# Kernel tuning notes

Hardware: AMD Instinct MI355X
Metric: run time of the kernel (lower is better)

The kernel has to match this reference:

```python
import jax, jax.numpy as jnp
import numpy as np

ITER = 50
HEADS = 8

def _ln(x, g, b, eps=1e-5):
    m = jnp.mean(x, -1, keepdims=True)
    v = jnp.var(x, -1, keepdims=True)
    return (x - m) * jax.lax.rsqrt(v + eps) * g + b

def _glu(x):
    a, b = jnp.split(x, 2, -1)
    return a * jax.nn.sigmoid(b)

def setup_inputs() -> dict:
    key = jax.random.key(0)
    ks = iter(jax.random.split(key, 48))
    B, D, E, M, H, O, NA, NO = 64, 2048, 512, 25, 32, 4096, 512, 512
    def nrm(shape, fan):
        return jax.random.normal(next(ks), shape, jnp.float32) / np.float32(np.sqrt(fan))
    return dict(
        x=jax.random.normal(next(ks), (B, 12, 8, 8), jnp.float32),
        kv_w=nrm((12, E), 12), kv_b=jnp.zeros(E), kv_ln_g=jnp.ones(E), kv_ln_b=jnp.zeros(E),
        q_w=nrm((NA, E), NA), q_b=jnp.zeros(E),
        wq=nrm((E, E), E), wk=nrm((E, E), E), wv=nrm((E, E), E), wo=nrm((E, E), E),
        bq=jnp.zeros(E), bk=jnp.zeros(E), bv=jnp.zeros(E), bo=jnp.zeros(E),
        syn_w=nrm((E + D, 2 * D), E + D), syn_b=jnp.zeros(2 * D),
        syn_ln_g=jnp.ones(D), syn_ln_b=jnp.zeros(D),
        nlm1_w=nrm((M, 2 * H, D), M), nlm1_b=jnp.zeros((D, 2 * H)),
        nlm2_w=nrm((H, 2, D), H), nlm2_b=jnp.zeros((D, 2)),
        start_activated_state=nrm((D,), D), start_trace=nrm((D, M), D + M),
        decay_action=jax.random.uniform(next(ks), (NA,)) * 0.5,
        decay_out=jax.random.uniform(next(ks), (NO,)) * 0.5,
        out_w=nrm((NO, O), NO), out_b=jnp.zeros(O),
        idx_a_left=jax.random.randint(next(ks), (NA,), 0, D, jnp.int32),
        idx_a_right=jax.random.randint(next(ks), (NA,), 0, D, jnp.int32),
        idx_o_left=jax.random.randint(next(ks), (NO,), 0, D, jnp.int32),
        idx_o_right=jax.random.randint(next(ks), (NO,), 0, D, jnp.int32),
    )

def reference(x, kv_w, kv_b, kv_ln_g, kv_ln_b, q_w, q_b, wq, wk, wv, wo, bq, bk, bv, bo,
              syn_w, syn_b, syn_ln_g, syn_ln_b, nlm1_w, nlm1_b, nlm2_w, nlm2_b,
              start_activated_state, start_trace, decay_action, decay_out, out_w, out_b,
              idx_a_left, idx_a_right, idx_o_left, idx_o_right):
    B = x.shape[0]
    D, M = start_trace.shape
    E = kv_w.shape[1]
    O = out_w.shape[1]
    Dh = E // HEADS
    # compute_features: backbone=none, pos=none -> flatten(2).transpose(1,2) then kv_proj
    feats = x.reshape(B, x.shape[1], -1).transpose(0, 2, 1)          # (B, 64, 12)
    kv = _ln(feats @ kv_w + kv_b, kv_ln_g, kv_ln_b)                  # (B, 64, E)
    kp = (kv @ wk + bk).reshape(B, -1, HEADS, Dh)                    # precompute K/V once
    vp = (kv @ wv + bv).reshape(B, -1, HEADS, Dh)
    r_a = jnp.exp(-jnp.clip(decay_action, 0.0, 15.0))
    r_o = jnp.exp(-jnp.clip(decay_out, 0.0, 15.0))
    trace0 = jnp.broadcast_to(start_trace, (B, D, M))
    act0 = jnp.broadcast_to(start_activated_state, (B, D))
    zA = jnp.zeros((B, decay_action.shape[0]))
    zO = jnp.zeros((B, decay_out.shape[0]))
    inv_sqrt_dh = np.float32(1.0 / np.sqrt(Dh))
    inv_log_o = np.float32(1.0 / np.log(O))

    def step(carry, _):
        trace, act, aA, bA, aO, bO = carry
        # action synchronisation (random-pairing: elementwise pair product, decayed)
        pw = act[:, idx_a_left] * act[:, idx_a_right]
        aA = r_a * aA + pw
        bA = r_a * bA + 1.0
        sync_a = aA * jax.lax.rsqrt(bA)
        # single-query MHA over the 64 board tokens
        q = sync_a @ q_w + q_b
        qh = (q @ wq + bq).reshape(B, HEADS, Dh)
        sc = jnp.einsum('bhd,bshd->bhs', qh, kp) * inv_sqrt_dh
        attn = jax.nn.softmax(sc, -1)
        o = jnp.einsum('bhs,bshd->bhd', attn, vp).reshape(B, E)
        attn_out = o @ wo + bo
        # synapse MLP (Linear -> GLU -> LayerNorm)
        pre = jnp.concatenate([attn_out, act], -1)
        state = _ln(_glu(pre @ syn_w + syn_b), syn_ln_g, syn_ln_b)   # (B, D)
        # shift memory trace and run per-neuron NLMs
        trace = jnp.concatenate([trace[:, :, 1:], state[:, :, None]], -1)
        h = _glu(jnp.einsum('bnm,mhn->bnh', trace, nlm1_w) + nlm1_b)
        act = _glu(jnp.einsum('bnm,mhn->bnh', h, nlm2_w) + nlm2_b)[..., 0]
        # output synchronisation + prediction + certainty
        pwo = act[:, idx_o_left] * act[:, idx_o_right]
        aO = r_o * aO + pwo
        bO = r_o * bO + 1.0
        sync_o = aO * jax.lax.rsqrt(bO)
        pred = sync_o @ out_w + out_b
        logp = jax.nn.log_softmax(pred, -1)
        ne = -jnp.sum(jnp.exp(logp) * logp, -1) * inv_log_o
        cert = jnp.stack([ne, 1.0 - ne], -1)
        return (trace, act, aA, bA, aO, bO), (pred, cert)

    _, (preds, certs) = jax.lax.scan(step, (trace0, act0, zA, zA, zO, zO), None, length=ITER)
    predictions = preds.transpose(1, 2, 0)   # (B, out_dims, iterations)
    certainties = certs.transpose(1, 2, 0)   # (B, 2, iterations)
    return predictions, certainties
```

## Files before the change

### kernel.cpp

```cpp
#include <hip/hip_runtime.h>
#include <math.h>

#define NB 64
#define ND 2048
#define NE 512
#define NM 25
#define NOUT 4096
#define NHEADS 8
#define NDH 64
#define NS 64
#define NITER 50
#define NKSYN 2560
#define PRED_TOTAL (NB * NOUT * NITER)

typedef unsigned short bf16_t;
typedef __attribute__((ext_vector_type(8))) short short8;
typedef __attribute__((ext_vector_type(4))) float f32x4;

__device__ __forceinline__ float sigm(float x) { return 1.f / (1.f + expf(-x)); }

__device__ __forceinline__ bf16_t f2bf(float f) {
    unsigned u = __float_as_uint(f);
    unsigned r = (u + 0x7FFFu + ((u >> 16) & 1u)) >> 16;
    return (bf16_t)r;
}
__device__ __forceinline__ float bf2f(bf16_t h) {
    return __uint_as_float(((unsigned)h) << 16);
}

__device__ __forceinline__ float wredsum(float v) {
#pragma unroll
    for (int o = 32; o; o >>= 1) v += __shfl_xor(v, o);
    return v;
}
__device__ __forceinline__ float wredmax(float v) {
#pragma unroll
    for (int o = 32; o; o >>= 1) v = fmaxf(v, __shfl_xor(v, o));
    return v;
}

template <int OP>
__device__ __forceinline__ float blockReduce(float v, float* red) {
    const int tid = threadIdx.x, lane = tid & 63, wid = tid >> 6;
    v = (OP == 0) ? wredsum(v) : wredmax(v);
    __syncthreads();
    if (lane == 0) red[wid] = v;
    __syncthreads();
    if (tid == 0) {
        const int nw = blockDim.x >> 6;
        float r = red[0];
        for (int w = 1; w < nw; ++w) r = (OP == 0) ? r + red[w] : fmaxf(r, red[w]);
        red[0] = r;
    }
    __syncthreads();
    return red[0];
}


__global__ __launch_bounds__(512) void k_fo(
        const float* __restrict__ actT, bf16_t* __restrict__ actB,
        float* __restrict__ aA, float* __restrict__ bA,
        const float* __restrict__ r_a,
        const int* __restrict__ ial, const int* __restrict__ iar,
        const bf16_t* __restrict__ W_qqb, const float* __restrict__ b_qq,
        const bf16_t* __restrict__ kvp,
        float* __restrict__ aO, float* __restrict__ bO,
        const float* __restrict__ r_o,
        const int* __restrict__ iol, const int* __restrict__ ior,
        const bf16_t* __restrict__ boutw, float* __restrict__ part_out,
        int doFront, int doOut, int it) {
    __shared__ float lds[8192];
    const int bid = blockIdx.x;
    const int t = threadIdx.x;
    const int lane = t & 63, wv = t >> 6;

    if (bid >= 256) {
        if (!doOut) return;
        const int itO = it - 1;
        const int srcO = itO & 1, dstO = srcO ^ 1;
        const int half = t >> 8, t2 = t & 255;
        const int unit = (bid - 256) * 2 + half;
        const int kp = unit >> 6, jt2 = unit & 63;
        float* sL = lds + half * 4096;
#pragma unroll
        for (int c = 0; c < 16; ++c) {
            const int idx = t2 + c * 256;
            const int il = idx >> 6, bb = idx & 63;
            const int i = kp * 64 + il;
            const float pl = actT[iol[i] * NB + bb];
            const float prr = actT[ior[i] * NB + bb];
            const float r = r_o[i];
            const float aN = r * aO[srcO * 32768 + i * NB + bb] + pl * prr;
            const float bN = r * bO[srcO * 32768 + i * NB + bb] + 1.f;
            if (jt2 == 0) {
                aO[dstO * 32768 + i * NB + bb] = aN;
                bO[dstO * 32768 + i * NB + bb] = bN;
            }
            sL[il * 64 + bb] = aN * rsqrtf(bN);
        }
        __syncthreads();
        const int bb = t2 & 63;
        const int j0 = jt2 * 64 + __builtin_amdgcn_readfirstlane((t2 >> 6) & 3) * 16;
        float acc[16];
#pragma unroll
        for (int q = 0; q < 16; ++q) acc[q] = 0.f;
#pragma unroll 4
        for (int k = 0; k < 64; ++k) {
            const float sv = sL[k * 64 + bb];
            const unsigned* wrow = (const unsigned*)(boutw + (size_t)(kp * 64 + k) * NOUT + j0);
#pragma unroll
            for (int q = 0; q < 8; ++q) {
                const unsigned u = wrow[q];
                const float w0 = __uint_as_float(u << 16);
                const float w1 = __uint_as_float(u & 0xffff0000u);
                acc[2 * q + 0] = fmaf(sv, w0, acc[2 * q + 0]);
                acc[2 * q + 1] = fmaf(sv, w1, acc[2 * q + 1]);
            }
        }
        float* dstp = part_out + ((size_t)(kp * NB + bb)) * NOUT + j0;
#pragma unroll
        for (int q = 0; q < 16; ++q) dstp[q] = acc[q];
        return;
    }

    if (!doFront) return;
    float* syncS = lds;
    float* partK = lds + 512;
    float* qhS = lds + 1024;
    float* attnS = lds + 1152;
    const int jt = bid >> 6, b = bid & 63;
    const int src = it & 1, dst = src ^ 1;
    {
        const int i = t;
        const float pl = actT[ial[i] * NB + b];
        const float prr = actT[iar[i] * NB + b];
        const float r = r_a[i];
        const float aN = r * aA[src * 32768 + b * NE + i] + pl * prr;
        const float bN = r * bA[src * 32768 + b * NE + i] + 1.f;
        if (jt == 0) {
            aA[dst * 32768 + b * NE + i] = aN;
            bA[dst * 32768 + b * NE + i] = bN;
        }
        syncS[i] = aN * rsqrtf(bN);
    }
    __syncthreads();
    {
        const int g = t >> 7, l = t & 127;
        const int j = jt * 128 + l;
        float acc = 0.f;
        const int kk0 = g * 128;
#pragma unroll 4
        for (int k = kk0; k < kk0 + 128; ++k)
            acc = fmaf(syncS[k], bf2f(W_qqb[k * NE + j]), acc);
        partK[g * 128 + l] = acc;
    }
    __syncthreads();
    if (t < 128) {
        qhS[t] = b_qq[jt * 128 + t] + partK[t] + partK[128 + t] + partK[256 + t] + partK[384 + t];
    }
    __syncthreads();
    if (wv < 2) {
        const int h = jt * 2 + wv, s = lane;
        const bf16_t* kpp = kvp + ((size_t)(b * NS + s) * 1024 + h * NDH);
        float sc = 0.f;
#pragma unroll 8
        for (int d = 0; d < NDH; ++d) sc = fmaf(qhS[wv * 64 + d], bf2f(kpp[d]), sc);
        sc *= 0.125f;
        const float mxv = wredmax(sc);
        const float ev = expf(sc - mxv);
        const float sm = wredsum(ev);
        attnS[wv * 64 + s] = ev / sm;
    }
    __syncthreads();
    if (wv < 2) {
        const int h = jt * 2 + wv, d = lane;
        const bf16_t* vpp = kvp + ((size_t)(b * NS) * 1024 + NE + h * NDH + d);
        float o = 0.f;
#pragma unroll 8
        for (int s2 = 0; s2 < NS; ++s2) o = fmaf(attnS[wv * 64 + s2], bf2f(vpp[(size_t)s2 * 1024]), o);
        actB[(size_t)b * NKSYN + h * NDH + d] = f2bf(o);
    }
}

__global__ __launch_bounds__(256) void k_gf(
        const bf16_t* __restrict__ actB, const bf16_t* __restrict__ bpack,
        float* __restrict__ part_syn,
        const float* __restrict__ part_out, const float* __restrict__ out_b,
        float* __restrict__ out, float* __restrict__ predTemp,
        int doGemm, int doFinal, int tt, int tmode) {
    __shared__ float red[8];
    const int bid = blockIdx.x;
    const int t = threadIdx.x;
    if (bid < 512) {
        if (!doGemm) return;
        const int kp = bid >> 6, jt = bid & 63;
        const int l = t & 63;
        const int wv = t >> 6;
        const int b0 = wv * 16;
        const int row = b0 + (l & 15);
        const int kgrp = l >> 4;
        f32x4 acc[4];
#pragma unroll
        for (int js = 0; js < 4; ++js) acc[js] = (f32x4){0.f, 0.f, 0.f, 0.f};
        const int ks0 = kp * 10;
#pragma unroll 2
        for (int ks = 0; ks < 10; ++ks) {
            const int kk = (ks0 + ks) * 32;
            const short8 av = *(const short8*)(actB + (size_t)row * NKSYN + kk + kgrp * 8);
#pragma unroll
            for (int js = 0; js < 4; ++js) {
                const short8 bv = *(const short8*)(bpack +
                    ((((size_t)(jt * 4 + js)) * 80 + ks0 + ks) * 64 + l) * 8);
                acc[js] = __builtin_amdgcn_mfma_f32_16x16x32_bf16(av, bv, acc[js], 0, 0, 0);
            }
        }
#pragma unroll
        for (int js = 0; js < 4; ++js) {
#pragma unroll
            for (int r = 0; r < 4; ++r) {
                const int b = b0 + kgrp * 4 + r;
                const int j = jt * 64 + js * 16 + (l & 15);
                part_syn[((size_t)(kp * NB + b)) * NOUT + j] = acc[js][r];
            }
        }
    } else {
        if (!doFinal) return;
        const int b = bid - 512;
        float pr[16];
        float lmax = -1e30f;
#pragma unroll
        for (int c = 0; c < 16; ++c) {
            const int j = t + c * 256;
            float v = out_b[j];
#pragma unroll
            for (int kp = 0; kp < 8; ++kp) v += part_out[((size_t)(kp * NB + b)) * NOUT + j];
            pr[c] = v;
            lmax = fmaxf(lmax, v);
        }
        const float mx = blockReduce<1>(lmax, red);
        float ls = 0.f;
#pragma unroll
        for (int c = 0; c < 16; ++c) ls += expf(pr[c] - mx);
        const float se = blockReduce<0>(ls, red);
        const float logZ = mx + logf(se);
        float le = 0.f;
#pragma unroll
        for (int c = 0; c < 16; ++c) { const float lp = pr[c] - logZ; le += expf(lp) * lp; }
        const float ent = blockReduce<0>(le, red);
        const float ne = -ent * 0.12022458674074694f;
        if (tmode) {
#pragma unroll
            for (int c = 0; c < 16; ++c)
                predTemp[((size_t)b * NITER + tt) * NOUT + t + c * 256] = pr[c];
        } else {
#pragma unroll
            for (int c = 0; c < 16; ++c) {
                const int j = t + c * 256;
                out[((size_t)b * NOUT + j) * NITER + tt] = pr[c];
            }
        }
        if (t == 0) {
            out[PRED_TOTAL + b * 100 + tt] = ne;
            out[PRED_TOTAL + b * 100 + 50 + tt] = 1.f - ne;
        }
    }
}

__global__ __launch_bounds__(512) void k_glu(const float* __restrict__ part,
                                             const float* __restrict__ sbe,
                                             float* __restrict__ trace2,
                                             float* __restrict__ statsPart, int pos) {
    __shared__ float red[8];
    const int b = blockIdx.x >> 2, q = blockIdx.x & 3;
    const int t = threadIdx.x;
    const int n = q * 512 + t;
    float ya = sbe[n], yb = sbe[n + ND];
#pragma unroll
    for (int kp = 0; kp < 8; ++kp) {
        ya += part[((size_t)(kp * NB + b)) * NOUT + n];
        yb += part[((size_t)(kp * NB + b)) * NOUT + n + ND];
    }
    const float g = ya * sigm(yb);
    trace2[((size_t)pos * ND + n) * NB + b] = g;
    const float s = blockReduce<0>(g, red);
    const float ss = blockReduce<0>(g * g, red);
    if (t == 0) {
        statsPart[(blockIdx.x) * 2 + 0] = s;
        statsPart[(blockIdx.x) * 2 + 1] = ss;
    }
}

__global__ __launch_bounds__(256) void k_nlm(float* __restrict__ trace2,
                                             const bf16_t* __restrict__ bw1t,
                                             const float* __restrict__ b1,
                                             const float* __restrict__ w2t,
                                             const float* __restrict__ b2,
                                             const float* __restrict__ statsPart,
                                             const float* __restrict__ ln_g,
                                             const float* __restrict__ ln_b,
                                             float* __restrict__ actT,
                                             bf16_t* __restrict__ actB, int pos) {
    __shared__ float sacc[32][64];
    __shared__ float pz[2][2][64];
    const int b = threadIdx.x & 63;
    const int g = __builtin_amdgcn_readfirstlane(threadIdx.x >> 6);
    const int n = blockIdx.x;
    const int hh0 = g * 16;
    float ssum = 0.f, ssq = 0.f;
#pragma unroll
    for (int q = 0; q < 4; ++q) {
        ssum += statsPart[(b * 4 + q) * 2 + 0];
        ssq  += statsPart[(b * 4 + q) * 2 + 1];
    }
    const float mean = ssum * (1.f / ND);
    const float rs = rsqrtf(ssq * (1.f / ND) - mean * mean + 1e-5f);

    float trv[NM];
    float trNew;
    {
        int phys = (pos + 1 < NM) ? pos + 1 : 0;
#pragma unroll
        for (int m = 0; m < NM - 1; ++m) {
            trv[m] = trace2[((size_t)phys * ND + n) * NB + b];
            phys = (phys + 1 < NM) ? phys + 1 : 0;
        }
        const float raw = trace2[((size_t)pos * ND + n) * NB + b];
        trNew = (raw - mean) * rs * ln_g[n] + ln_b[n];
        trv[NM - 1] = trNew;
    }
    __syncthreads();
    if (g == 0) trace2[((size_t)pos * ND + n) * NB + b] = trNew;

    float acc[16];
    {
        const float* brow = b1 + n * 64 + hh0;
#pragma unroll
        for (int q = 0; q < 16; ++q) acc[q] = brow[q];
    }
#pragma unroll
    for (int m = 0; m < NM; ++m) {
        const float tr = trv[m];
        const unsigned* wrow = (const unsigned*)(bw1t + ((size_t)n * NM + m) * 64 + hh0);
#pragma unroll
        for (int q = 0; q < 8; ++q) {
            const unsigned u = wrow[q];
            const float w0 = __uint_as_float(u << 16);
            const float w1 = __uint_as_float(u & 0xffff0000u);
            acc[2 * q + 0] = fmaf(tr, w0, acc[2 * q + 0]);
            acc[2 * q + 1] = fmaf(tr, w1, acc[2 * q + 1]);
        }
    }
    if (g >= 2) {
#pragma unroll
        for (int q = 0; q < 16; ++q) sacc[hh0 - 32 + q][b] = acc[q];
    }
    __syncthreads();
    if (g < 2) {
        const float* w2r = w2t + n * 64;
        float z0p = 0.f, z1p = 0.f;
#pragma unroll
        for (int q = 0; q < 16; ++q) {
            const int i = hh0 + q;
            const float hv = acc[q] * sigm(sacc[i][b]);
            z0p = fmaf(hv, w2r[i], z0p);
            z1p = fmaf(hv, w2r[32 + i], z1p);
        }
        pz[0][g][b] = z0p;
        pz[1][g][b] = z1p;
    }
    __syncthreads();
    if (g == 0) {
        const float z0 = b2[n * 2 + 0] + pz[0][0][b] + pz[0][1][b];
        const float z1 = b2[n * 2 + 1] + pz[1][0][b] + pz[1][1][b];
        const float val = z0 * sigm(z1);
        actT[n * NB + b] = val;
        actB[(size_t)b * NKSYN + NE + n] = f2bf(val);
    }
}


__global__ __launch_bounds__(256) void k_p0(const float* __restrict__ dec_a,
                                            const float* __restrict__ dec_o,
                                            const float* __restrict__ q_b,
                                            const float* __restrict__ wq,
                                            const float* __restrict__ bq,
                                            float* __restrict__ r_a, float* __restrict__ r_o,
                                            float* __restrict__ b_qq) {
    const int t = threadIdx.x;
    if (blockIdx.x == 0) {
        for (int i = t; i < NE; i += 256) {
            r_a[i] = expf(-fminf(fmaxf(dec_a[i], 0.f), 15.f));
            r_o[i] = expf(-fminf(fmaxf(dec_o[i], 0.f), 15.f));
        }
        return;
    }
    __shared__ float partial[4][64];
    const int c = (blockIdx.x - 1) * 64 + (t & 63);
    const int kg = t >> 6;
    float acc = 0.f;
#pragma unroll 4
    for (int k = kg * 128; k < kg * 128 + 128; ++k)
        acc = fmaf(q_b[k], wq[k * NE + c], acc);
    partial[kg][t & 63] = acc;
    __syncthreads();
    if (t < 64) {
        const int cc = (blockIdx.x - 1) * 64 + t;
        b_qq[cc] = bq[cc] + partial[0][t] + partial[1][t] + partial[2][t] + partial[3][t];
    }
}

__global__ __launch_bounds__(256) void k_packB(const float* __restrict__ src,
                                               int ld, int nbj, int ksgs,
                                               bf16_t* __restrict__ dst) {
    __shared__ float tile[32][65];
    const int ksg = blockIdx.x / nbj;
    const int bj = blockIdx.x % nbj;
    const int k0 = ksg * 32, j0 = bj * 64;
    for (int i = threadIdx.x; i < 2048; i += 256) {
        const int kk = i >> 6, jj = i & 63;
        tile[kk][jj] = src[(size_t)(k0 + kk) * ld + j0 + jj];
    }
    __syncthreads();
    for (int i = threadIdx.x; i < 2048; i += 256) {
        const int j16 = i >> 9;
        const int ii = i & 511;
        const int e = ii & 7, l = ii >> 3;
        const int kk = (l >> 4) * 8 + e;
        const int jj = j16 * 16 + (l & 15);
        dst[(((size_t)(bj * 4 + j16) * ksgs + ksg) * 64) * 8 + ii] = f2bf(tile[kk][jj]);
    }
}

__global__ __launch_bounds__(256, 2) void k_woSynM(const bf16_t* __restrict__ bwo,
                                                   const bf16_t* __restrict__ synw0p,
                                                   float* __restrict__ woSyn) {
    const int mt = blockIdx.x >> 6, nt = blockIdx.x & 63;
    const int l = threadIdx.x & 63;
    const int w = threadIdx.x >> 6;
    const int row0 = mt * 64 + w * 16;
    const int row = row0 + (l & 15);
    const int kgrp = l >> 4;
    f32x4 acc[4];
#pragma unroll
    for (int js = 0; js < 4; ++js) acc[js] = (f32x4){0.f, 0.f, 0.f, 0.f};
#pragma unroll 2
    for (int ks = 0; ks < 16; ++ks) {
        const short8 av = *(const short8*)(bwo + (size_t)row * NE + ks * 32 + kgrp * 8);
#pragma unroll
        for (int js = 0; js < 4; ++js) {
            const short8 bv8 = *(const short8*)(synw0p +
                ((((size_t)(nt * 4 + js)) * 16 + ks) * 64 + l) * 8);
            acc[js] = __builtin_amdgcn_mfma_f32_16x16x32_bf16(av, bv8, acc[js], 0, 0, 0);
        }
    }
#pragma unroll
    for (int js = 0; js < 4; ++js) {
#pragma unroll
        for (int r = 0; r < 4; ++r) {
            const int e = row0 + kgrp * 4 + r;
            const int c = nt * 64 + js * 16 + (l & 15);
            woSyn[(size_t)e * NOUT + c] = acc[js][r];
        }
    }
}

__global__ __launch_bounds__(256, 2) void k_wqqM(const bf16_t* __restrict__ bqw,
                                                 const bf16_t* __restrict__ wqp,
                                                 bf16_t* __restrict__ W_qqb) {
    const int mt = blockIdx.x >> 3, nt = blockIdx.x & 7;
    const int l = threadIdx.x & 63;
    const int w = threadIdx.x >> 6;
    const int row0 = mt * 64 + w * 16;
    const int row = row0 + (l & 15);
    const int kgrp = l >> 4;
    f32x4 acc[4];
#pragma unroll
    for (int js = 0; js < 4; ++js) acc[js] = (f32x4){0.f, 0.f, 0.f, 0.f};
#pragma unroll 2
    for (int ks = 0; ks < 16; ++ks) {
        const short8 av = *(const short8*)(bqw + (size_t)row * NE + ks * 32 + kgrp * 8);
#pragma unroll
        for (int js = 0; js < 4; ++js) {
            const short8 bv8 = *(const short8*)(wqp +
                ((((size_t)(nt * 4 + js)) * 16 + ks) * 64 + l) * 8);
            acc[js] = __builtin_amdgcn_mfma_f32_16x16x32_bf16(av, bv8, acc[js], 0, 0, 0);
        }
    }
#pragma unroll
    for (int js = 0; js < 4; ++js) {
#pragma unroll
        for (int r = 0; r < 4; ++r) {
            const int e = row0 + kgrp * 4 + r;
            const int c = nt * 64 + js * 16 + (l & 15);
            W_qqb[(size_t)e * NE + c] = f2bf(acc[js][r]);
        }
    }
}

__global__ __launch_bounds__(256) void k_sbe(const float* __restrict__ syn_b,
                                             const float* __restrict__ bo,
                                             const float* __restrict__ syn_w,
                                             float* __restrict__ sbe) {
    __shared__ float partial[4][64];
    const int c = blockIdx.x * 64 + (threadIdx.x & 63);
    const int kg = threadIdx.x >> 6;
    float acc = 0.f;
#pragma unroll 4
    for (int jp = kg * 128; jp < kg * 128 + 128; ++jp)
        acc = fmaf(bo[jp], syn_w[(size_t)jp * NOUT + c], acc);
    partial[kg][threadIdx.x & 63] = acc;
    __syncthreads();
    if (threadIdx.x < 64) {
        const int cc = blockIdx.x * 64 + threadIdx.x;
        sbe[cc] = syn_b[cc] + partial[0][threadIdx.x] + partial[1][threadIdx.x]
                + partial[2][threadIdx.x] + partial[3][threadIdx.x];
    }
}

__global__ __launch_bounds__(256) void k_cvt(const float* __restrict__ s,
                                             bf16_t* __restrict__ d) {
    const size_t i = (size_t)blockIdx.x * 256 + threadIdx.x;
    d[i] = f2bf(s[i]);
}

__global__ __launch_bounds__(256) void k_bpack(const float* __restrict__ woSyn,
                                               const float* __restrict__ syn_w,
                                               bf16_t* __restrict__ bpack) {
    __shared__ float tile[32][65];
    const int ksg = blockIdx.x >> 6;
    const int bj = blockIdx.x & 63;
    const int k0 = ksg * 32, j0 = bj * 64;
    for (int i = threadIdx.x; i < 2048; i += 256) {
        const int kk = i >> 6, jj = i & 63;
        const int k = k0 + kk;
        tile[kk][jj] = (k < NE) ? woSyn[(size_t)k * NOUT + j0 + jj]
                                : syn_w[(size_t)k * NOUT + j0 + jj];
    }
    __syncthreads();
    for (int i = threadIdx.x; i < 2048; i += 256) {
        const int j16 = i >> 9;
        const int ii = i & 511;
        const int e = ii & 7, l = ii >> 3;
        const int kk = (l >> 4) * 8 + e;
        const int jj = j16 * 16 + (l & 15);
        bpack[(((size_t)(bj * 4 + j16) * 80 + ksg) * 64) * 8 + ii] = f2bf(tile[kk][jj]);
    }
}

__global__ __launch_bounds__(256) void k_wkvpack(const float* __restrict__ wk,
                                                 const float* __restrict__ wv,
                                                 bf16_t* __restrict__ wkvpack) {
    __shared__ float tile[32][65];
    const int ksg = blockIdx.x >> 4;
    const int bj = blockIdx.x & 15;
    const int k0 = ksg * 32, j0 = bj * 64;
    for (int i = threadIdx.x; i < 2048; i += 256) {
        const int kk = i >> 6, jj = i & 63;
        const int k = k0 + kk, j = j0 + jj;
        tile[kk][jj] = (j < NE) ? wk[(size_t)k * NE + j] : wv[(size_t)k * NE + (j - NE)];
    }
    __syncthreads();
    for (int i = threadIdx.x; i < 2048; i += 256) {
        const int j16 = i >> 9;
        const int ii = i & 511;
        const int e = ii & 7, l = ii >> 3;
        const int kk = (l >> 4) * 8 + e;
        const int jj = j16 * 16 + (l & 15);
        wkvpack[(((size_t)(bj * 4 + j16) * 16 + ksg) * 64) * 8 + ii] = f2bf(tile[kk][jj]);
    }
}

__global__ __launch_bounds__(256) void k_init_trace2(const float* __restrict__ st,
                                                     float* __restrict__ trace2) {
    const int idx = blockIdx.x * 256 + threadIdx.x;
    const int n = (idx >> 6) & (ND - 1);
    const int m = idx >> 17;
    trace2[idx] = st[n * NM + m];
}

#define INIT_TOTAL (NB * ND + 8 * NB * NE)
__global__ __launch_bounds__(256) void k_init_state(const float* __restrict__ sa,
                                                    float* __restrict__ actT,
                                                    bf16_t* __restrict__ actB,
                                                    float* __restrict__ zeroBase) {
    const int idx = blockIdx.x * 256 + threadIdx.x;
    if (idx >= INIT_TOTAL) return;
    if (idx < NB * ND) {
        const int b = idx & 63, n = idx >> 6;
        actT[n * NB + b] = sa[n];
        actB[(size_t)b * NKSYN + NE + n] = f2bf(sa[n]);
    } else {
        zeroBase[idx - NB * ND] = 0.f;
    }
}

__global__ __launch_bounds__(512) void k_p1a(const float* __restrict__ x,
                                             const float* __restrict__ kv_w,
                                             const float* __restrict__ kv_b,
                                             const float* __restrict__ ln_g,
                                             const float* __restrict__ ln_b,
                                             bf16_t* __restrict__ kvnB) {
    __shared__ float kvT[NE][17];
    __shared__ float mS[16], rS[16];
    const int b = blockIdx.x >> 2, s0 = (blockIdx.x & 3) * 16;
    const int t = threadIdx.x;
    const int lane = t & 63, wvi = t >> 6;
    {
        float w[12];
#pragma unroll
        for (int c = 0; c < 12; ++c) w[c] = kv_w[c * NE + t];
        const float kb = kv_b[t];
#pragma unroll
        for (int tok = 0; tok < 16; ++tok) {
            float acc = kb;
#pragma unroll
            for (int c = 0; c < 12; ++c)
                acc = fmaf(x[b * 768 + c * 64 + s0 + tok], w[c], acc);
            kvT[t][tok] = acc;
        }
    }
    __syncthreads();
#pragma unroll
    for (int q = 0; q < 2; ++q) {
        const int tok = wvi * 2 + q;
        float s = 0.f, ss = 0.f;
#pragma unroll
        for (int i = 0; i < 8; ++i) {
            const float v = kvT[lane + 64 * i][tok];
            s += v; ss = fmaf(v, v, ss);
        }
        s = wredsum(s); ss = wredsum(ss);
        if (lane == 0) {
            const float mean = s * (1.f / NE);
            mS[tok] = mean;
            rS[tok] = rsqrtf(ss * (1.f / NE) - mean * mean + 1e-5f);
        }
    }
    __syncthreads();
    {
        const float g = ln_g[t], bb2 = ln_b[t];
#pragma unroll
        for (int tok = 0; tok < 16; ++tok) {
            const float kvn = (kvT[t][tok] - mS[tok]) * rS[tok] * g + bb2;
            kvnB[(size_t)(b * 64 + s0 + tok) * NE + t] = f2bf(kvn);
        }
    }
}

__global__ __launch_bounds__(256, 2) void k_p1b(const bf16_t* __restrict__ kvnB,
                                                const bf16_t* __restrict__ wkvpack,
                                                const float* __restrict__ bk,
                                                const float* __restrict__ bv,
                                                bf16_t* __restrict__ kvp) {
    const int mt = blockIdx.x >> 4, nt = blockIdx.x & 15;
    const int l = threadIdx.x & 63;
    const int wv = threadIdx.x >> 6;
    const int row0 = mt * 64 + wv * 16;
    const int row = row0 + (l & 15);
    const int kgrp = l >> 4;
    f32x4 acc[4];
#pragma unroll
    for (int js = 0; js < 4; ++js) acc[js] = (f32x4){0.f, 0.f, 0.f, 0.f};
#pragma unroll 2
    for (int ks = 0; ks < 16; ++ks) {
        const short8 av = *(const short8*)(kvnB + (size_t)row * NE + ks * 32 + kgrp * 8);
#pragma unroll
        for (int js = 0; js < 4; ++js) {
            const short8 bv8 = *(const short8*)(wkvpack +
                ((((size_t)(nt * 4 + js)) * 16 + ks) * 64 + l) * 8);
            acc[js] = __builtin_amdgcn_mfma_f32_16x16x32_bf16(av, bv8, acc[js], 0, 0, 0);
        }
    }
#pragma unroll
    for (int js = 0; js < 4; ++js) {
#pragma unroll
        for (int r = 0; r < 4; ++r) {
            const int tok = row0 + kgrp * 4 + r;
            const int j = nt * 64 + js * 16 + (l & 15);
            const float bias = (j < NE) ? bk[j] : bv[j - NE];
            kvp[(size_t)tok * 1024 + j] = f2bf(acc[js][r] + bias);
        }
    }
}

__global__ __launch_bounds__(256) void k_w1t(const float* __restrict__ w1,
                                             bf16_t* __restrict__ bw1t) {
    __shared__ float tile[64][65];
    const int m = blockIdx.x >> 5, n0 = (blockIdx.x & 31) << 6;
    for (int i = threadIdx.x; i < 4096; i += 256) {
        const int hh = i >> 6, nn = i & 63;
        tile[hh][nn] = w1[(size_t)(m * 64 + hh) * ND + n0 + nn];
    }
    __syncthreads();
    for (int i = threadIdx.x; i < 4096; i += 256) {
        const int nn = i >> 6, hh = i & 63;
        bw1t[((size_t)(n0 + nn) * NM + m) * 64 + hh] = f2bf(tile[hh][nn]);
    }
}

__global__ __launch_bounds__(256) void k_w2t(const float* __restrict__ w2,
                                             float* __restrict__ w2t) {
    const int idx = blockIdx.x * 256 + threadIdx.x;
    const int i = idx & 31;
    const int c = (idx >> 5) & 1;
    const int n = idx >> 6;
    w2t[idx] = w2[(size_t)(i * 2 + c) * ND + n];
}

__global__ __launch_bounds__(256) void k_transpose(const float* __restrict__ predTemp,
                                                   float* __restrict__ out) {
    __shared__ float tile[NS * NITER];
    const int b = blockIdx.x >> 6;
    const int j0 = (blockIdx.x & 63) * 64;
    for (int i = threadIdx.x; i < 3200; i += 256) {
        const int tt = i >> 6, jj = i & 63;
        tile[jj * NITER + tt] = predTemp[((size_t)b * NITER + tt) * NOUT + j0 + jj];
    }
    __syncthreads();
    float* dst = out + ((size_t)b * NOUT + j0) * NITER;
    for (int i = threadIdx.x; i < 3200; i += 256) dst[i] = tile[i];
}

extern "C" void kernel_launch(void* const* d_in, const int* in_sizes, int n_in,
                              void* d_out, int out_size, void* d_ws, size_t ws_size,
                              hipStream_t stream) {
    const float* x        = (const float*)d_in[0];
    const float* kv_w     = (const float*)d_in[1];
    const float* kv_b     = (const float*)d_in[2];
    const float* kv_ln_g  = (const float*)d_in[3];
    const float* kv_ln_b  = (const float*)d_in[4];
    const float* q_w      = (const float*)d_in[5];
    const float* q_b      = (const float*)d_in[6];
    const float* wq       = (const float*)d_in[7];
    const float* wk       = (const float*)d_in[8];
    const float* wv       = (const float*)d_in[9];
    const float* wo       = (const float*)d_in[10];
    const float* bq       = (const float*)d_in[11];
    const float* bk       = (const float*)d_in[12];
    const float* bv       = (const float*)d_in[13];
    const float* bo       = (const float*)d_in[14];
    const float* syn_w    = (const float*)d_in[15];
    const float* syn_b    = (const float*)d_in[16];
    const float* syn_ln_g = (const float*)d_in[17];
    const float* syn_ln_b = (const float*)d_in[18];
    const float* nlm1_w   = (const float*)d_in[19];
    const float* nlm1_b   = (const float*)d_in[20];
    const float* nlm2_w   = (const float*)d_in[21];
    const float* nlm2_b   = (const float*)d_in[22];
    const float* start_a  = (const float*)d_in[23];
    const float* start_tr = (const float*)d_in[24];
    const float* dec_a    = (const float*)d_in[25];
    const float* dec_o    = (const float*)d_in[26];
    const float* out_w    = (const float*)d_in[27];
    const float* out_b    = (const float*)d_in[28];
    const int* ial        = (const int*)d_in[29];
    const int* iar        = (const int*)d_in[30];
    const int* iol        = (const int*)d_in[31];
    const int* ior        = (const int*)d_in[32];
    float* out = (float*)d_out;

    float* ws = (float*)d_ws;
    size_t off = 0;
    auto alloc = [&](size_t n) { float* p = ws + off; off += n; return p; };
    float* actT      = alloc((size_t)ND * NB);
    bf16_t* actB     = (bf16_t*)alloc((size_t)NB * NKSYN / 2);
    bf16_t* kvnB     = (bf16_t*)alloc((size_t)NB * NS * NE / 2);
    bf16_t* kvp      = (bf16_t*)alloc((size_t)NB * NS * 1024 / 2);
    bf16_t* wkvpack  = (bf16_t*)alloc((size_t)NE * 1024 / 2);
    bf16_t* W_qqb    = (bf16_t*)alloc((size_t)NE * NE / 2);
    bf16_t* boutw    = (bf16_t*)alloc((size_t)NE * NOUT / 2);
    bf16_t* bwo      = (bf16_t*)alloc((size_t)NE * NE / 2);
    bf16_t* bqw      = (bf16_t*)alloc((size_t)NE * NE / 2);
    bf16_t* synw0p   = (bf16_t*)alloc((size_t)NE * NOUT / 2);
    bf16_t* wqp      = (bf16_t*)alloc((size_t)NE * NE / 2);
    float* woSyn     = alloc((size_t)NE * NOUT);
    bf16_t* bpack    = (bf16_t*)alloc((size_t)NKSYN * NOUT / 2);
    float* sbe       = alloc(NOUT);
    float* b_qq      = alloc(NE);
    float* r_a       = alloc(NE);
    float* r_o       = alloc(NE);
    float* statsPart = alloc(512);
    float* aA        = alloc((size_t)2 * NB * NE);
    float* bA        = alloc((size_t)2 * NB * NE);
    float* aO        = alloc((size_t)2 * NB * NE);
    float* bO        = alloc((size_t)2 * NB * NE);
    float* trace2    = alloc((size_t)NM * ND * NB);
    float* part_syn  = alloc((size_t)8 * NB * NOUT);
    float* part_out  = alloc((size_t)8 * NB * NOUT);
    bf16_t* bw1t     = (bf16_t*)alloc((size_t)ND * NM * 64 / 2);
    float* w2t       = alloc((size_t)ND * 64);
    int tmode = 0;
    float* predTemp = nullptr;
    if ((off + (size_t)PRED_TOTAL) * sizeof(float) <= ws_size) {
        predTemp = alloc((size_t)PRED_TOTAL);
        tmode = 1;
    }

    k_p0<<<9, 256, 0, stream>>>(dec_a, dec_o, q_b, wq, bq, r_a, r_o, b_qq);
    k_cvt<<<(NE * NE) / 256, 256, 0, stream>>>(wo, bwo);
    k_cvt<<<(NE * NE) / 256, 256, 0, stream>>>(q_w, bqw);
    k_packB<<<16 * 64, 256, 0, stream>>>(syn_w, NOUT, 64, 16, synw0p);
    k_packB<<<16 * 8, 256, 0, stream>>>(wq, NE, 8, 16, wqp);
    k_woSynM<<<512, 256, 0, stream>>>(bwo, synw0p, woSyn);
    k_wqqM<<<64, 256, 0, stream>>>(bqw, wqp, W_qqb);
    k_sbe<<<64, 256, 0, stream>>>(syn_b, bo, syn_w, sbe);
    k_bpack<<<5120, 256, 0, stream>>>(woSyn, syn_w, bpack);
    k_wkvpack<<<256, 256, 0, stream>>>(wk, wv, wkvpack);
    k_cvt<<<(NE * NOUT) / 256, 256, 0, stream>>>(out_w, boutw);
    k_init_trace2<<<(NM * ND * NB) / 256, 256, 0, stream>>>(start_tr, trace2);
    k_init_state<<<(INIT_TOTAL + 255) / 256, 256, 0, stream>>>(start_a, actT, actB, aA);
    k_p1a<<<256, 512, 0, stream>>>(x, kv_w, kv_b, kv_ln_g, kv_ln_b, kvnB);
    k_p1b<<<1024, 256, 0, stream>>>(kvnB, wkvpack, bk, bv, kvp);
    k_w1t<<<800, 256, 0, stream>>>(nlm1_w, bw1t);
    k_w2t<<<(ND * 64) / 256, 256, 0, stream>>>(nlm2_w, w2t);

    for (int t = 0; t < NITER; ++t) {
        k_fo<<<512, 512, 0, stream>>>(actT, actB, aA, bA, r_a, ial, iar, W_qqb, b_qq,
                                      kvp, aO, bO, r_o, iol, ior, boutw, part_out,
                                      1, (t > 0) ? 1 : 0, t);
        k_gf<<<576, 256, 0, stream>>>(actB, bpack, part_syn, part_out, out_b, out, predTemp,
                                      1, (t > 0) ? 1 : 0, t - 1, tmode);
        k_glu<<<256, 512, 0, stream>>>(part_syn, sbe, trace2, statsPart, t % NM);
        k_nlm<<<2048, 256, 0, stream>>>(trace2, bw1t, nlm1_b, w2t, nlm2_b, statsPart,
                                        syn_ln_g, syn_ln_b, actT, actB, t % NM);
    }
    k_fo<<<512, 512, 0, stream>>>(actT, actB, aA, bA, r_a, ial, iar, W_qqb, b_qq,
                                  kvp, aO, bO, r_o, iol, ior, boutw, part_out,
                                  0, 1, NITER);
    k_gf<<<576, 256, 0, stream>>>(actB, bpack, part_syn, part_out, out_b, out, predTemp,
                                  0, 1, NITER - 1, tmode);
    if (tmode) k_transpose<<<NB * 64, 256, 0, stream>>>(predTemp, out);
}
```

Before: 2.957 ms.

## Move output projection to MFMA bf16 GEMM and shift softmax finalize into GLU kernel

```diff
diff --git a/kernel.cpp b/kernel.cpp
--- a/kernel.cpp
+++ b/kernel.cpp
@@ -67,59 +67,32 @@
         float* __restrict__ aO, float* __restrict__ bO,
         const float* __restrict__ r_o,
         const int* __restrict__ iol, const int* __restrict__ ior,
-        const bf16_t* __restrict__ boutw, float* __restrict__ part_out,
+        bf16_t* __restrict__ syncB,
         int doFront, int doOut, int it) {
-    __shared__ float lds[8192];
+    __shared__ float lds[1280];
     const int bid = blockIdx.x;
     const int t = threadIdx.x;
     const int lane = t & 63, wv = t >> 6;
 
     if (bid >= 256) {
         if (!doOut) return;
+        const int sb = bid - 256;
         const int itO = it - 1;
         const int srcO = itO & 1, dstO = srcO ^ 1;
-        const int half = t >> 8, t2 = t & 255;
-        const int unit = (bid - 256) * 2 + half;
-        const int kp = unit >> 6, jt2 = unit & 63;
-        float* sL = lds + half * 4096;
-#pragma unroll
-        for (int c = 0; c < 16; ++c) {
-            const int idx = t2 + c * 256;
+#pragma unroll
+        for (int c = 0; c < 8; ++c) {
+            const int idx = t + c * 512;
             const int il = idx >> 6, bb = idx & 63;
-            const int i = kp * 64 + il;
+            const int i = sb * 64 + il;
             const float pl = actT[iol[i] * NB + bb];
             const float prr = actT[ior[i] * NB + bb];
             const float r = r_o[i];
             const float aN = r * aO[srcO * 32768 + i * NB + bb] + pl * prr;
             const float bN = r * bO[srcO * 32768 + i * NB + bb] + 1.f;
-            if (jt2 == 0) {
-                aO[dstO * 32768 + i * NB + bb] = aN;
-                bO[dstO * 32768 + i * NB + bb] = bN;
-            }
-            sL[il * 64 + bb] = aN * rsqrtf(bN);
-        }
-        __syncthreads();
-        const int bb = t2 & 63;
-        const int j0 = jt2 * 64 + __builtin_amdgcn_readfirstlane((t2 >> 6) & 3) * 16;
-        float acc[16];
-#pragma unroll
-        for (int q = 0; q < 16; ++q) acc[q] = 0.f;
-#pragma unroll 4
-        for (int k = 0; k < 64; ++k) {
-            const float sv = sL[k * 64 + bb];
-            const unsigned* wrow = (const unsigned*)(boutw + (size_t)(kp * 64 + k) * NOUT + j0);
-#pragma unroll
-            for (int q = 0; q < 8; ++q) {
-                const unsigned u = wrow[q];
-                const float w0 = __uint_as_float(u << 16);
-                const float w1 = __uint_as_float(u & 0xffff0000u);
-                acc[2 * q + 0] = fmaf(sv, w0, acc[2 * q + 0]);
-                acc[2 * q + 1] = fmaf(sv, w1, acc[2 * q + 1]);
-            }
-        }
-        float* dstp = part_out + ((size_t)(kp * NB + bb)) * NOUT + j0;
-#pragma unroll
-        for (int q = 0; q < 16; ++q) dstp[q] = acc[q];
+            aO[dstO * 32768 + i * NB + bb] = aN;
+            bO[dstO * 32768 + i * NB + bb] = bN;
+            syncB[(size_t)bb * NE + i] = f2bf(aN * rsqrtf(bN));
+        }
         return;
     }
 
@@ -185,10 +158,9 @@
 __global__ __launch_bounds__(256) void k_gf(
         const bf16_t* __restrict__ actB, const bf16_t* __restrict__ bpack,
         float* __restrict__ part_syn,
-        const float* __restrict__ part_out, const float* __restrict__ out_b,
-        float* __restrict__ out, float* __restrict__ predTemp,
-        int doGemm, int doFinal, int tt, int tmode) {
-    __shared__ float red[8];
+        const bf16_t* __restrict__ syncB, const bf16_t* __restrict__ outwp,
+        const float* __restrict__ out_b, float* __restrict__ predRaw,
+        int doGemm, int doOutM) {
     const int bid = blockIdx.x;
     const int t = threadIdx.x;
     if (bid < 512) {
@@ -224,38 +196,98 @@
             }
         }
     } else {
+        if (!doOutM) return;
+        const int nt = bid - 512;
+        const int l = t & 63;
+        const int w = t >> 6;
+        const int row0 = w * 16;
+        const int row = row0 + (l & 15);
+        const int kgrp = l >> 4;
+        f32x4 acc[4];
+#pragma unroll
+        for (int js = 0; js < 4; ++js) acc[js] = (f32x4){0.f, 0.f, 0.f, 0.f};
+#pragma unroll 2
+        for (int ks = 0; ks < 16; ++ks) {
+            const short8 av = *(const short8*)(syncB + (size_t)row * NE + ks * 32 + kgrp * 8);
+#pragma unroll
+            for (int js = 0; js < 4; ++js) {
+                const short8 bv8 = *(const short8*)(outwp +
+                    ((((size_t)(nt * 4 + js)) * 16 + ks) * 64 + l) * 8);
+                acc[js] = __builtin_amdgcn_mfma_f32_16x16x32_bf16(av, bv8, acc[js], 0, 0, 0);
+            }
+        }
+#pragma unroll
+        for (int js = 0; js < 4; ++js) {
+#pragma unroll
+            for (int r = 0; r < 4; ++r) {
+                const int b = row0 + kgrp * 4 + r;
+                const int j = nt * 64 + js * 16 + (l & 15);
+                predRaw[(size_t)b * NOUT + j] = acc[js][r] + out_b[j];
+            }
+        }
+    }
+}
+
+__global__ __launch_bounds__(512) void k_glu(const float* __restrict__ part,
+                                             const float* __restrict__ sbe,
+                                             float* __restrict__ trace2,
+                                             float* __restrict__ statsPart, int pos,
+                                             const float* __restrict__ predRaw,
+                                             float* __restrict__ out,
+                                             float* __restrict__ predTemp,
+                                             int doGlu, int doFinal, int tt, int tmode) {
+    __shared__ float red[8];
+    const int bid = blockIdx.x;
+    const int t = threadIdx.x;
+    if (bid < 256) {
+        if (!doGlu) return;
+        const int b = bid >> 2, q = bid & 3;
+        const int n = q * 512 + t;
+        float ya = sbe[n], yb = sbe[n + ND];
+#pragma unroll
+        for (int kp = 0; kp < 8; ++kp) {
+            ya += part[((size_t)(kp * NB + b)) * NOUT + n];
+            yb += part[((size_t)(kp * NB + b)) * NOUT + n + ND];
+        }
+        const float g = ya * sigm(yb);
+        trace2[((size_t)pos * ND + n) * NB + b] = g;
+        const float s = blockReduce<0>(g, red);
+        const float ss = blockReduce<0>(g * g, red);
+        if (t == 0) {
+            statsPart[bid * 2 + 0] = s;
+            statsPart[bid * 2 + 1] = ss;
+        }
+    } else {
         if (!doFinal) return;
-        const int b = bid - 512;
-        float pr[16];
+        const int b = bid - 256;
+        float pr[8];
         float lmax = -1e30f;
 #pragma unroll
-        for (int c = 0; c < 16; ++c) {
-            const int j = t + c * 256;
-            float v = out_b[j];
-#pragma unroll
-            for (int kp = 0; kp < 8; ++kp) v += part_out[((size_t)(kp * NB + b)) * NOUT + j];
+        for (int c = 0; c < 8; ++c) {
+            const int j = t + c * 512;
+            const float v = predRaw[(size_t)b * NOUT + j];
             pr[c] = v;
             lmax = fmaxf(lmax, v);
         }
         const float mx = blockReduce<1>(lmax, red);
         float ls = 0.f;
 #pragma unroll
-        for (int c = 0; c < 16; ++c) ls += expf(pr[c] - mx);
+        for (int c = 0; c < 8; ++c) ls += expf(pr[c] - mx);
         const float se = blockReduce<0>(ls, red);
         const float logZ = mx + logf(se);
         float le = 0.f;
 #pragma unroll
-        for (int c = 0; c < 16; ++c) { const float lp = pr[c] - logZ; le += expf(lp) * lp; }
+        for (int c = 0; c < 8; ++c) { const float lp = pr[c] - logZ; le += expf(lp) * lp; }
         const float ent = blockReduce<0>(le, red);
         const float ne = -ent * 0.12022458674074694f;
         if (tmode) {
 #pragma unroll
-            for (int c = 0; c < 16; ++c)
-                predTemp[((size_t)b * NITER + tt) * NOUT + t + c * 256] = pr[c];
+            for (int c = 0; c < 8; ++c)
+                predTemp[((size_t)b * NITER + tt) * NOUT + t + c * 512] = pr[c];
         } else {
 #pragma unroll
-            for (int c = 0; c < 16; ++c) {
-                const int j = t + c * 256;
+            for (int c = 0; c < 8; ++c) {
+                const int j = t + c * 512;
                 out[((size_t)b * NOUT + j) * NITER + tt] = pr[c];
             }
         }
@@ -263,30 +295,6 @@
             out[PRED_TOTAL + b * 100 + tt] = ne;
             out[PRED_TOTAL + b * 100 + 50 + tt] = 1.f - ne;
         }
-    }
-}
-
-__global__ __launch_bounds__(512) void k_glu(const float* __restrict__ part,
-                                             const float* __restrict__ sbe,
-                                             float* __restrict__ trace2,
-                                             float* __restrict__ statsPart, int pos) {
-    __shared__ float red[8];
-    const int b = blockIdx.x >> 2, q = blockIdx.x & 3;
-    const int t = threadIdx.x;
-    const int n = q * 512 + t;
-    float ya = sbe[n], yb = sbe[n + ND];
-#pragma unroll
-    for (int kp = 0; kp < 8; ++kp) {
-        ya += part[((size_t)(kp * NB + b)) * NOUT + n];
-        yb += part[((size_t)(kp * NB + b)) * NOUT + n + ND];
-    }
-    const float g = ya * sigm(yb);
-    trace2[((size_t)pos * ND + n) * NB + b] = g;
-    const float s = blockReduce<0>(g, red);
-    const float ss = blockReduce<0>(g * g, red);
-    if (t == 0) {
-        statsPart[(blockIdx.x) * 2 + 0] = s;
-        statsPart[(blockIdx.x) * 2 + 1] = ss;
     }
 }
 
@@ -768,11 +776,12 @@
     bf16_t* kvp      = (bf16_t*)alloc((size_t)NB * NS * 1024 / 2);
     bf16_t* wkvpack  = (bf16_t*)alloc((size_t)NE * 1024 / 2);
     bf16_t* W_qqb    = (bf16_t*)alloc((size_t)NE * NE / 2);
-    bf16_t* boutw    = (bf16_t*)alloc((size_t)NE * NOUT / 2);
+    bf16_t* outwp    = (bf16_t*)alloc((size_t)NE * NOUT / 2);
     bf16_t* bwo      = (bf16_t*)alloc((size_t)NE * NE / 2);
     bf16_t* bqw      = (bf16_t*)alloc((size_t)NE * NE / 2);
     bf16_t* synw0p   = (bf16_t*)alloc((size_t)NE * NOUT / 2);
     bf16_t* wqp      = (bf16_t*)alloc((size_t)NE * NE / 2);
+    bf16_t* syncB    = (bf16_t*)alloc((size_t)NB * NE / 2);
     float* woSyn     = alloc((size_t)NE * NOUT);
     bf16_t* bpack    = (bf16_t*)alloc((size_t)NKSYN * NOUT / 2);
     float* sbe       = alloc(NOUT);
@@ -786,7 +795,7 @@
     float* bO        = alloc((size_t)2 * NB * NE);
     float* trace2    = alloc((size_t)NM * ND * NB);
     float* part_syn  = alloc((size_t)8 * NB * NOUT);
-    float* part_out  = alloc((size_t)8 * NB * NOUT);
+    float* predRaw   = alloc((size_t)NB * NOUT);
     bf16_t* bw1t     = (bf16_t*)alloc((size_t)ND * NM * 64 / 2);
     float* w2t       = alloc((size_t)ND * 64);
     int tmode = 0;
@@ -801,12 +810,12 @@
     k_cvt<<<(NE * NE) / 256, 256, 0, stream>>>(q_w, bqw);
     k_packB<<<16 * 64, 256, 0, stream>>>(syn_w, NOUT, 64, 16, synw0p);
     k_packB<<<16 * 8, 256, 0, stream>>>(wq, NE, 8, 16, wqp);
+    k_packB<<<16 * 64, 256, 0, stream>>>(out_w, NOUT, 64, 16, outwp);
     k_woSynM<<<512, 256, 0, stream>>>(bwo, synw0p, woSyn);
     k_wqqM<<<64, 256, 0, stream>>>(bqw, wqp, W_qqb);
     k_sbe<<<64, 256, 0, stream>>>(syn_b, bo, syn_w, sbe);
     k_bpack<<<5120, 256, 0, stream>>>(woSyn, syn_w, bpack);
     k_wkvpack<<<256, 256, 0, stream>>>(wk, wv, wkvpack);
-    k_cvt<<<(NE * NOUT) / 256, 256, 0, stream>>>(out_w, boutw);
     k_init_trace2<<<(NM * ND * NB) / 256, 256, 0, stream>>>(start_tr, trace2);
     k_init_state<<<(INIT_TOTAL + 255) / 256, 256, 0, stream>>>(start_a, actT, actB, aA);
     k_p1a<<<256, 512, 0, stream>>>(x, kv_w, kv_b, kv_ln_g, kv_ln_b, kvnB);
@@ -815,19 +824,23 @@
     k_w2t<<<(ND * 64) / 256, 256, 0, stream>>>(nlm2_w, w2t);
 
     for (int t = 0; t < NITER; ++t) {
-        k_fo<<<512, 512, 0, stream>>>(actT, actB, aA, bA, r_a, ial, iar, W_qqb, b_qq,
-                                      kvp, aO, bO, r_o, iol, ior, boutw, part_out,
-                                      1, (t > 0) ? 1 : 0, t);
-        k_gf<<<576, 256, 0, stream>>>(actB, bpack, part_syn, part_out, out_b, out, predTemp,
-                                      1, (t > 0) ? 1 : 0, t - 1, tmode);
-        k_glu<<<256, 512, 0, stream>>>(part_syn, sbe, trace2, statsPart, t % NM);
+        const int prev = (t > 0) ? 1 : 0;
+        k_fo<<<264, 512, 0, stream>>>(actT, actB, aA, bA, r_a, ial, iar, W_qqb, b_qq,
+                                      kvp, aO, bO, r_o, iol, ior, syncB,
+                                      1, prev, t);
+        k_gf<<<576, 256, 0, stream>>>(actB, bpack, part_syn, syncB, outwp, out_b, predRaw,
+                                      1, prev);
+        k_glu<<<320, 512, 0, stream>>>(part_syn, sbe, trace2, statsPart, t % NM,
+                                       predRaw, out, predTemp, 1, prev, t - 1, tmode);
         k_nlm<<<2048, 256, 0, stream>>>(trace2, bw1t, nlm1_b, w2t, nlm2_b, statsPart,
                                         syn_ln_g, syn_ln_b, actT, actB, t % NM);
     }
-    k_fo<<<512, 512, 0, stream>>>(actT, actB, aA, bA, r_a, ial, iar, W_qqb, b_qq,
-                                  kvp, aO, bO, r_o, iol, ior, boutw, part_out,
+    k_fo<<<264, 512, 0, stream>>>(actT, actB, aA, bA, r_a, ial, iar, W_qqb, b_qq,
+                                  kvp, aO, bO, r_o, iol, ior, syncB,
                                   0, 1, NITER);
-    k_gf<<<576, 256, 0, stream>>>(actB, bpack, part_syn, part_out, out_b, out, predTemp,
-                                  0, 1, NITER - 1, tmode);
+    k_gf<<<576, 256, 0, stream>>>(actB, bpack, part_syn, syncB, outwp, out_b, predRaw,
+                                  0, 1);
+    k_glu<<<320, 512, 0, stream>>>(part_syn, sbe, trace2, statsPart, 0,
+                                   predRaw, out, predTemp, 0, 1, NITER - 1, tmode);
     if (tmode) k_transpose<<<NB * 64, 256, 0, stream>>>(predTemp, out);
 }
```

Result: faster. 2.815 ms (-4.8%).
